# Kernel optimization log

Hardware: AMD Instinct MI355X
Metric: run time of the kernel (lower is better)

## Reference

```python
import jax, jax.numpy as jnp
import numpy as np

B, S, D, H, HG, W, DFF = 2, 4096, 1024, 16, 2, 128, 4096
NEG = -1e30  # stands in for -inf in the original masking (exp underflows to exactly 0)


def _chunk(x, w):
    # overlapping chunks of size 2w with hop w (tf.signal.frame equivalent)
    b, s, d = x.shape
    blocks = x.reshape(b, s // w, w, d)
    return jnp.concatenate([blocks[:, :-1], blocks[:, 1:]], axis=2)  # [b, s//w-1, 2w, d]


def _sliding_scores(q, k, w):
    # q,k: [BH, S, dh] (q pre-scaled). Returns banded scores [BH, S, 2w+1].
    bh, s, d = q.shape
    c = s // w - 1
    attn = jnp.einsum('bcxd,bcyd->bcxy', _chunk(q, w), _chunk(k, w))  # [bh,c,2w,2w]
    # pad one row then reshape: the skew trick from the source (_pad_and_transpose_last_two_dims)
    dca = jnp.pad(attn, ((0, 0), (0, 0), (0, 1), (0, 0))).reshape(bh, c, 2 * w, 2 * w + 1)
    up = jnp.concatenate([dca[:, :, :w, :w + 1], dca[:, -1:, w:, :w + 1]], axis=1)          # [bh,c+1,w,w+1]
    first = jnp.roll(dca, shift=(1, w), axis=(2, 3))[:, :1, :w, :w]                          # first-chunk lower triangle
    low = jnp.concatenate([first, dca[:, :, -(w + 1):-1, w + 1:]], axis=1)                   # [bh,c+1,w,w]
    return jnp.concatenate([low, up], axis=-1).reshape(bh, s, 2 * w + 1)


def _invalid_mask(s, w):
    # _mask_invalid_locations: mask band positions that fall outside [0, S)
    m = jnp.tril(jnp.ones((w, w + 1), jnp.float32))[::-1]
    m = jnp.pad(m, ((0, s - w), (0, w)))
    return (m + m[::-1, ::-1]) > 0  # [s, 2w+1]


def _sliding_value(p, v, w):
    # p: [BH, S, 2w+1] band probs, v: [BH, S, dh] -> [BH, S, dh]
    bh, s, kk = p.shape
    d = v.shape[-1]
    c = s // w
    cp = jnp.pad(p.reshape(bh, c, w, kk), ((0, 0), (0, 0), (0, 0), (0, w + 1)))
    # pad-and-diagonalize skew: row r shifted right by r -> aligns band with 3w value window
    cp = cp.reshape(bh, c, w * (3 * w + 2))[:, :, :-w].reshape(bh, c, w, 3 * w + 1)[:, :, :, :-1]
    pv = jnp.pad(v, ((0, 0), (w, w), (0, 0))).reshape(bh, c + 2, w, d)
    cv = jnp.concatenate([pv[:, :-2], pv[:, 1:-1], pv[:, 2:]], axis=2)  # [bh,c,3w,d]
    return jnp.einsum('bcwk,bckd->bcwd', cp, cv).reshape(bh, s, d)


def _layernorm(x, g, b):
    mu = jnp.mean(x, -1, keepdims=True)
    var = jnp.mean(jnp.square(x - mu), -1, keepdims=True)
    return (x - mu) * jax.lax.rsqrt(var + 1e-6) * g + b


def setup_inputs() -> dict:
    key = jax.random.key(0)
    ks = jax.random.split(key, 8)
    dense = lambda k, i, o: 0.02 * jax.random.normal(k, (i, o), jnp.float32)
    return {
        'x': jax.random.normal(ks[0], (B, S, D), jnp.float32),
        'mask': jnp.zeros((B, 1, 1, S), jnp.float32),
        'wq_k': dense(ks[1], D, D), 'wq_b': jnp.zeros((D,), jnp.float32),
        'wk_k': dense(ks[2], D, D), 'wk_b': jnp.zeros((D,), jnp.float32),
        'wv_k': dense(ks[3], D, D), 'wv_b': jnp.zeros((D,), jnp.float32),
        'wo_k': dense(ks[4], D, D), 'wo_b': jnp.zeros((D,), jnp.float32),
        'ffn_w1': dense(ks[5], D, DFF), 'ffn_b1': jnp.zeros((DFF,), jnp.float32),
        'ffn_w2': dense(ks[6], DFF, D), 'ffn_b2': jnp.zeros((D,), jnp.float32),
        'ln1_g': jnp.ones((D,), jnp.float32), 'ln1_b': jnp.zeros((D,), jnp.float32),
        'ln2_g': jnp.ones((D,), jnp.float32), 'ln2_b': jnp.zeros((D,), jnp.float32),
    }


def reference(x, mask, wq_k, wq_b, wk_k, wk_b, wv_k, wv_b, wo_k, wo_b,
              ffn_w1, ffn_b1, ffn_w2, ffn_b2, ln1_g, ln1_b, ln2_g, ln2_b):
    dh = D // H
    hl = H - HG
    split = lambda t: t.reshape(B, S, H, dh).transpose(0, 2, 1, 3)  # [B,H,S,dh]
    q, k, v = split(x @ wq_k + wq_b), split(x @ wk_k + wk_b), split(x @ wv_k + wv_b)
    scale = 1.0 / jnp.sqrt(jnp.float32(dh))
    # ---- local (sliding-window) heads ----
    ql = (q[:, :hl] * scale).reshape(B * hl, S, dh)
    kl = k[:, :hl].reshape(B * hl, S, dh)
    vl = v[:, :hl].reshape(B * hl, S, dh)
    scores = _sliding_scores(ql, kl, W)
    scores = jnp.where(_invalid_mask(S, W)[None], NEG, scores)
    out_l = _sliding_value(jax.nn.softmax(scores, axis=-1), vl, W).reshape(B, hl, S, dh)
    # ---- global heads (full attention, graph_mask=None branch) ----
    logits = jnp.einsum('bhqd,bhkd->bhqk', q[:, hl:], k[:, hl:]) * scale + mask * (-1000.0)
    out_g = jnp.einsum('bhqk,bhkd->bhqd', jax.nn.softmax(logits, axis=-1), v[:, hl:])
    # ---- merge heads, output proj, residual + LN, FFN (leaky_relu alpha=0.2 = tf default) ----
    attn = jnp.concatenate([out_l, out_g], axis=1).transpose(0, 2, 1, 3).reshape(B, S, D)
    out1 = _layernorm(x + attn @ wo_k + wo_b, ln1_g, ln1_b)
    h = jax.nn.leaky_relu(out1 @ ffn_w1 + ffn_b1, negative_slope=0.2)
    return _layernorm(out1 + h @ ffn_w2 + ffn_b2, ln2_g, ln2_b)
```

## Files before the change

### kernel.cpp

```cpp
#include <hip/hip_runtime.h>
#include <hip/hip_bf16.h>

typedef unsigned short u16;
typedef unsigned int u32;
typedef __attribute__((ext_vector_type(8))) short short8;
typedef __attribute__((ext_vector_type(8))) unsigned short ushort8v;
typedef __attribute__((ext_vector_type(4))) unsigned short ushort4v;
typedef __attribute__((ext_vector_type(4))) float f32x4;

static constexpr int B_ = 2, S_ = 4096, D_ = 1024, H_ = 16, HG_ = 2, W_ = 128, DFF_ = 4096;
static constexpr int HL_ = H_ - HG_;
static constexpr int M_ = B_ * S_;
static constexpr int NCH_ = 4;

static __device__ __forceinline__ u16 f2b(float f) {
    u32 u = __builtin_bit_cast(u32, f);
    u32 r = (u + 0x7fffu + ((u >> 16) & 1u)) >> 16;
    return (u16)r;
}
static __device__ __forceinline__ float b2f(u16 b) {
    return __builtin_bit_cast(float, (u32)b << 16);
}

__global__ __launch_bounds__(256) void k_f32_to_bf16(const float* __restrict__ src,
                                                     u16* __restrict__ dst, int n4) {
    int i = blockIdx.x * 256 + threadIdx.x;
    if (i >= n4) return;
    float4 v = reinterpret_cast<const float4*>(src)[i];
    ushort4v o; o[0] = f2b(v.x); o[1] = f2b(v.y); o[2] = f2b(v.z); o[3] = f2b(v.w);
    reinterpret_cast<ushort4v*>(dst)[i] = o;
}

__global__ __launch_bounds__(256) void k_transpose_bf16(const float* __restrict__ src,
                                                        u16* __restrict__ dst,
                                                        int K, int N, int ro) {
    __shared__ float tile[32][33];
    const int tx = threadIdx.x & 31, ty = threadIdx.x >> 5;
    const int bx = blockIdx.x, by = blockIdx.y;
#pragma unroll
    for (int jj = 0; jj < 4; ++jj) {
        int kk = by * 32 + ty + jj * 8;
        int nn = bx * 32 + tx;
        tile[ty + jj * 8][tx] = src[(size_t)kk * N + nn];
    }
    __syncthreads();
#pragma unroll
    for (int jj = 0; jj < 4; ++jj) {
        int nn = bx * 32 + ty + jj * 8;
        int kk = by * 32 + tx;
        dst[(size_t)(ro + nn) * K + kk] = f2b(tile[tx][ty + jj * 8]);
    }
}

__global__ __launch_bounds__(256) void k_transpose_v(const u16* __restrict__ qkv,
                                                     u16* __restrict__ vT) {
    __shared__ u16 tile[32][33];
    const int tx = threadIdx.x & 31, ty = threadIdx.x >> 5;
    const int s0 = blockIdx.x * 32;
    const int d0 = blockIdx.y * 32;
    const int bh = blockIdx.z;
    const int b = bh >> 4, h = bh & 15;
#pragma unroll
    for (int jj = 0; jj < 4; ++jj) {
        int srow = s0 + ty + jj * 8;
        tile[ty + jj * 8][tx] = qkv[(size_t)(b * S_ + srow) * 3072 + 2048 + h * 64 + d0 + tx];
    }
    __syncthreads();
#pragma unroll
    for (int jj = 0; jj < 4; ++jj) {
        int d = d0 + ty + jj * 8;
        vT[(size_t)((b * H_ + h) * 64 + d) * S_ + s0 + tx] = tile[tx][ty + jj * 8];
    }
}

__global__ void k_pack_bias3(const float* __restrict__ a, const float* __restrict__ b,
                             const float* __restrict__ c, float* __restrict__ dst) {
    int i = blockIdx.x * 256 + threadIdx.x;
    if (i >= 3072) return;
    dst[i] = i < 1024 ? a[i] : (i < 2048 ? b[i - 1024] : c[i - 2048]);
}

#define GLDS16(gp, lp) __builtin_amdgcn_global_load_lds( \
    (const __attribute__((address_space(1))) void*)(gp),  \
    (__attribute__((address_space(3))) void*)(lp), 16, 0, 0)

template <bool LEAKY, bool OUTF, bool OUTB>
__global__ __launch_bounds__(256) void k_gemm(const u16* __restrict__ A, const u16* __restrict__ Bt,
                                              const float* __restrict__ bias,
                                              float* __restrict__ Cf, u16* __restrict__ Cb,
                                              int M, int N, int K) {
    __shared__ __align__(16) u16 lA[128 * 32];
    __shared__ __align__(16) u16 lB[128 * 32];
    const int tid = threadIdx.x;
    const int lane = tid & 63, wave = tid >> 6;
    const int wr = wave >> 1, wc = wave & 1;
    const int m0 = blockIdx.x * 128, n0 = blockIdx.y * 128;

    f32x4 acc[4][4];
#pragma unroll
    for (int i = 0; i < 4; ++i)
#pragma unroll
        for (int j = 0; j < 4; ++j)
#pragma unroll
            for (int e = 0; e < 4; ++e) acc[i][j][e] = 0.f;

    const int arow = tid >> 2;
    const int acol = (tid & 3) * 8;
    const int koff = (lane >> 4) * 8;
    const int rbase = wr * 64 + (lane & 15);
    const int cbase = wc * 64 + (lane & 15);

    for (int k0 = 0; k0 < K; k0 += 32) {
        __syncthreads();
        {
            const u16* ga0 = A + (size_t)(m0 + arow) * K + k0 + acol;
            const u16* ga1 = A + (size_t)(m0 + 64 + arow) * K + k0 + acol;
            GLDS16(ga0, lA + wave * 512);
            GLDS16(ga1, lA + 2048 + wave * 512);
            const u16* gb0 = Bt + (size_t)(n0 + arow) * K + k0 + acol;
            const u16* gb1 = Bt + (size_t)(n0 + 64 + arow) * K + k0 + acol;
            GLDS16(gb0, lB + wave * 512);
            GLDS16(gb1, lB + 2048 + wave * 512);
        }
        __syncthreads();

        short8 af[4], bfr[4];
#pragma unroll
        for (int mi = 0; mi < 4; ++mi)
            af[mi] = *reinterpret_cast<const short8*>(&lA[(rbase + mi * 16) * 32 + koff]);
#pragma unroll
        for (int ni = 0; ni < 4; ++ni)
            bfr[ni] = *reinterpret_cast<const short8*>(&lB[(cbase + ni * 16) * 32 + koff]);
        __builtin_amdgcn_s_setprio(1);
#pragma unroll
        for (int mi = 0; mi < 4; ++mi)
#pragma unroll
            for (int ni = 0; ni < 4; ++ni)
                acc[mi][ni] = __builtin_amdgcn_mfma_f32_16x16x32_bf16(af[mi], bfr[ni], acc[mi][ni], 0, 0, 0);
        __builtin_amdgcn_s_setprio(0);
    }

#pragma unroll
    for (int mi = 0; mi < 4; ++mi) {
        const int rowb = m0 + wr * 64 + mi * 16 + (lane >> 4) * 4;
#pragma unroll
        for (int ni = 0; ni < 4; ++ni) {
            const int col = n0 + wc * 64 + ni * 16 + (lane & 15);
            const float bs = bias[col];
#pragma unroll
            for (int j = 0; j < 4; ++j) {
                float v = acc[mi][ni][j] + bs;
                if (LEAKY) v = v > 0.f ? v : 0.2f * v;
                const size_t idx = (size_t)(rowb + j) * N + col;
                if (OUTF) Cf[idx] = v;
                if (OUTB) Cb[idx] = f2b(v);
            }
        }
    }
}

__global__ __launch_bounds__(256) void k_attn_local(const u16* __restrict__ qkv,
                                                    const u16* __restrict__ vT,
                                                    u16* __restrict__ out) {
    __shared__ __align__(16) u16 Kl[64][72];
    __shared__ __align__(16) u16 Vl[64][72];
    __shared__ __align__(16) u16 Pl[4][1024];
    const int tid = threadIdx.x, lane = tid & 63, wave = tid >> 6;
    const int c = lane & 15, g = lane >> 4;
    const int b = blockIdx.z, h = blockIdx.y;
    const int q0 = blockIdx.x * 64;
    const int qrow = q0 + wave * 16 + c;

    short8 qf[2];
    {
        const u16* qp = qkv + (size_t)(b * S_ + qrow) * 3072 + h * 64 + g * 8;
        qf[0] = *reinterpret_cast<const short8*>(qp);
        qf[1] = *reinterpret_cast<const short8*>(qp + 32);
    }

    f32x4 acc[4];
#pragma unroll
    for (int dt = 0; dt < 4; ++dt)
#pragma unroll
        for (int j = 0; j < 4; ++j) acc[dt][j] = 0.f;
    float mrow = -1e30f, lrow = 0.f;

    const int t_lo = max(0, q0 - W_) >> 6;
    const int t_hi = min(S_ - 1, q0 + 63 + W_) >> 6;
    u16* pw = Pl[wave];

    for (int t = t_lo; t <= t_hi; ++t) {
        __syncthreads();
#pragma unroll
        for (int it = 0; it < 2; ++it) {
            int L = it * 256 + tid;
            int r = L >> 3, cb = (L & 7) * 8;
            *reinterpret_cast<ushort8v*>(&Kl[r][cb]) =
                *reinterpret_cast<const ushort8v*>(&qkv[(size_t)(b * S_ + t * 64 + r) * 3072 + 1024 + h * 64 + cb]);
            *reinterpret_cast<ushort8v*>(&Vl[r][cb]) =
                *reinterpret_cast<const ushort8v*>(&vT[(size_t)((b * H_ + h) * 64 + r) * S_ + t * 64 + cb]);
        }
        __syncthreads();

        f32x4 s[4];
#pragma unroll
        for (int nt = 0; nt < 4; ++nt)
#pragma unroll
            for (int j = 0; j < 4; ++j) s[nt][j] = 0.f;
        __builtin_amdgcn_s_setprio(1);
#pragma unroll
        for (int kc = 0; kc < 2; ++kc) {
#pragma unroll
            for (int nt = 0; nt < 4; ++nt) {
                short8 kf = *reinterpret_cast<const short8*>(&Kl[nt * 16 + c][kc * 32 + g * 8]);
                s[nt] = __builtin_amdgcn_mfma_f32_16x16x32_bf16(kf, qf[kc], s[nt], 0, 0, 0);
            }
        }
        __builtin_amdgcn_s_setprio(0);

        float p[4][4];
        float tmax = -1e30f;
#pragma unroll
        for (int nt = 0; nt < 4; ++nt)
#pragma unroll
            for (int j = 0; j < 4; ++j) {
                float sv = s[nt][j] * 0.125f;
                int key = t * 64 + nt * 16 + 4 * g + j;
                bool val = (key >= qrow - W_) && (key <= qrow + W_);
                sv = val ? sv : -1e30f;
                p[nt][j] = sv;
                tmax = fmaxf(tmax, sv);
            }
        tmax = fmaxf(tmax, __shfl_xor(tmax, 16));
        tmax = fmaxf(tmax, __shfl_xor(tmax, 32));
        float mnew = fmaxf(mrow, tmax);
        float fac = __expf(mrow - mnew);
        mrow = mnew;
        float psum = 0.f;
#pragma unroll
        for (int nt = 0; nt < 4; ++nt)
#pragma unroll
            for (int j = 0; j < 4; ++j) {
                p[nt][j] = __expf(p[nt][j] - mnew);
                psum += p[nt][j];
            }
        lrow = lrow * fac + psum;
#pragma unroll
        for (int dt = 0; dt < 4; ++dt)
#pragma unroll
            for (int j = 0; j < 4; ++j) acc[dt][j] *= fac;

#pragma unroll
        for (int nt = 0; nt < 4; ++nt)
#pragma unroll
            for (int jp = 0; jp < 2; ++jp) {
                u32 pk = (u32)f2b(p[nt][2 * jp]) | ((u32)f2b(p[nt][2 * jp + 1]) << 16);
                int byteoff = (c << 7) + ((nt * 32 + 8 * g + 4 * jp) ^ ((c & 7) << 4));
                *reinterpret_cast<u32*>(reinterpret_cast<char*>(pw) + byteoff) = pk;
            }
        asm volatile("s_waitcnt lgkmcnt(0)" ::: "memory");

        __builtin_amdgcn_s_setprio(1);
#pragma unroll
        for (int h2 = 0; h2 < 2; ++h2) {
            int rb = (c << 7) + ((h2 * 64 + g * 16) ^ ((c & 7) << 4));
            short8 pa = *reinterpret_cast<const short8*>(reinterpret_cast<char*>(pw) + rb);
#pragma unroll
            for (int dt = 0; dt < 4; ++dt) {
                short8 vf = *reinterpret_cast<const short8*>(&Vl[dt * 16 + c][h2 * 32 + g * 8]);
                acc[dt] = __builtin_amdgcn_mfma_f32_16x16x32_bf16(vf, pa, acc[dt], 0, 0, 0);
            }
        }
        __builtin_amdgcn_s_setprio(0);
    }

    float lfull = lrow + __shfl_xor(lrow, 16);
    lfull += __shfl_xor(lfull, 32);
    const float rinv = 1.0f / lfull;

#pragma unroll
    for (int dt = 0; dt < 4; ++dt) {
        u32 w0 = (u32)f2b(acc[dt][0] * rinv) | ((u32)f2b(acc[dt][1] * rinv) << 16);
        u32 w1 = (u32)f2b(acc[dt][2] * rinv) | ((u32)f2b(acc[dt][3] * rinv) << 16);
        uint2 wv; wv.x = w0; wv.y = w1;
        *reinterpret_cast<uint2*>(out + (size_t)(b * S_ + qrow) * 1024 + h * 64 + dt * 16 + 4 * g) = wv;
    }
}

__global__ __launch_bounds__(256) void k_attn_global_part(const u16* __restrict__ qkv,
                                                          const u16* __restrict__ vT,
                                                          const float* __restrict__ mask,
                                                          float* __restrict__ po,
                                                          float* __restrict__ ml) {
    __shared__ __align__(16) u16 Kl[64][72];
    __shared__ __align__(16) u16 Vl[64][72];
    __shared__ __align__(16) u16 Pl[4][1024];
    __shared__ float maskl[64];
    const int tid = threadIdx.x, lane = tid & 63, wave = tid >> 6;
    const int c = lane & 15, g = lane >> 4;
    const int b = blockIdx.z;
    const int hh = blockIdx.y >> 2, ch = blockIdx.y & 3;
    const int h = HL_ + hh;
    const int q0 = blockIdx.x * 64;
    const int qrow = q0 + wave * 16 + c;

    short8 qf[2];
    {
        const u16* qp = qkv + (size_t)(b * S_ + qrow) * 3072 + h * 64 + g * 8;
        qf[0] = *reinterpret_cast<const short8*>(qp);
        qf[1] = *reinterpret_cast<const short8*>(qp + 32);
    }

    f32x4 acc[4];
#pragma unroll
    for (int dt = 0; dt < 4; ++dt)
#pragma unroll
        for (int j = 0; j < 4; ++j) acc[dt][j] = 0.f;
    float mrow = -1e30f, lrow = 0.f;
    u16* pw = Pl[wave];

    const int t_lo = ch * (S_ / 64 / NCH_), t_hi = t_lo + (S_ / 64 / NCH_) - 1;
    for (int t = t_lo; t <= t_hi; ++t) {
        __syncthreads();
#pragma unroll
        for (int it = 0; it < 2; ++it) {
            int L = it * 256 + tid;
            int r = L >> 3, cb = (L & 7) * 8;
            *reinterpret_cast<ushort8v*>(&Kl[r][cb]) =
                *reinterpret_cast<const ushort8v*>(&qkv[(size_t)(b * S_ + t * 64 + r) * 3072 + 1024 + h * 64 + cb]);
            *reinterpret_cast<ushort8v*>(&Vl[r][cb]) =
                *reinterpret_cast<const ushort8v*>(&vT[(size_t)((b * H_ + h) * 64 + r) * S_ + t * 64 + cb]);
        }
        if (tid < 64) maskl[tid] = mask[b * S_ + t * 64 + tid] * (-1000.0f);
        __syncthreads();

        f32x4 s[4];
#pragma unroll
        for (int nt = 0; nt < 4; ++nt)
#pragma unroll
            for (int j = 0; j < 4; ++j) s[nt][j] = 0.f;
        __builtin_amdgcn_s_setprio(1);
#pragma unroll
        for (int kc = 0; kc < 2; ++kc) {
#pragma unroll
            for (int nt = 0; nt < 4; ++nt) {
                short8 kf = *reinterpret_cast<const short8*>(&Kl[nt * 16 + c][kc * 32 + g * 8]);
                s[nt] = __builtin_amdgcn_mfma_f32_16x16x32_bf16(kf, qf[kc], s[nt], 0, 0, 0);
            }
        }
        __builtin_amdgcn_s_setprio(0);

        float p[4][4];
        float tmax = -1e30f;
#pragma unroll
        for (int nt = 0; nt < 4; ++nt)
#pragma unroll
            for (int j = 0; j < 4; ++j) {
                float sv = s[nt][j] * 0.125f + maskl[nt * 16 + 4 * g + j];
                p[nt][j] = sv;
                tmax = fmaxf(tmax, sv);
            }
        tmax = fmaxf(tmax, __shfl_xor(tmax, 16));
        tmax = fmaxf(tmax, __shfl_xor(tmax, 32));
        float mnew = fmaxf(mrow, tmax);
        float fac = __expf(mrow - mnew);
        mrow = mnew;
        float psum = 0.f;
#pragma unroll
        for (int nt = 0; nt < 4; ++nt)
#pragma unroll
            for (int j = 0; j < 4; ++j) {
                p[nt][j] = __expf(p[nt][j] - mnew);
                psum += p[nt][j];
            }
        lrow = lrow * fac + psum;
#pragma unroll
        for (int dt = 0; dt < 4; ++dt)
#pragma unroll
            for (int j = 0; j < 4; ++j) acc[dt][j] *= fac;

#pragma unroll
        for (int nt = 0; nt < 4; ++nt)
#pragma unroll
            for (int jp = 0; jp < 2; ++jp) {
                u32 pk = (u32)f2b(p[nt][2 * jp]) | ((u32)f2b(p[nt][2 * jp + 1]) << 16);
                int byteoff = (c << 7) + ((nt * 32 + 8 * g + 4 * jp) ^ ((c & 7) << 4));
                *reinterpret_cast<u32*>(reinterpret_cast<char*>(pw) + byteoff) = pk;
            }
        asm volatile("s_waitcnt lgkmcnt(0)" ::: "memory");

        __builtin_amdgcn_s_setprio(1);
#pragma unroll
        for (int h2 = 0; h2 < 2; ++h2) {
            int rb = (c << 7) + ((h2 * 64 + g * 16) ^ ((c & 7) << 4));
            short8 pa = *reinterpret_cast<const short8*>(reinterpret_cast<char*>(pw) + rb);
#pragma unroll
            for (int dt = 0; dt < 4; ++dt) {
                short8 vf = *reinterpret_cast<const short8*>(&Vl[dt * 16 + c][h2 * 32 + g * 8]);
                acc[dt] = __builtin_amdgcn_mfma_f32_16x16x32_bf16(vf, pa, acc[dt], 0, 0, 0);
            }
        }
        __builtin_amdgcn_s_setprio(0);
    }

    float lfull = lrow + __shfl_xor(lrow, 16);
    lfull += __shfl_xor(lfull, 32);

    float* po_blk = po + ((((size_t)(b * HG_ + hh) * NCH_ + ch) * (S_ / 64) + blockIdx.x) * 4096);
    const int ql = wave * 16 + c;
#pragma unroll
    for (int dt = 0; dt < 4; ++dt)
        *reinterpret_cast<f32x4*>(po_blk + ql * 64 + dt * 16 + 4 * g) = acc[dt];
    if (g == 0) {
        size_t mb = (((size_t)(b * HG_ + hh) * NCH_ + ch) * S_ + q0 + ql) * 2;
        ml[mb] = mrow;
        ml[mb + 1] = lfull;
    }
}

__global__ __launch_bounds__(256) void k_attn_merge(const float* __restrict__ po,
                                                    const float* __restrict__ ml,
                                                    u16* __restrict__ out) {
    const int qb = blockIdx.x, hh = blockIdx.y, b = blockIdx.z;
    const int t = threadIdx.x;
    const int ql = t >> 2, d0 = (t & 3) * 16;
    const int q = qb * 64 + ql;

    float mv[NCH_], lv[NCH_];
    float M = -1e30f;
#pragma unroll
    for (int ch = 0; ch < NCH_; ++ch) {
        size_t mb = (((size_t)(b * HG_ + hh) * NCH_ + ch) * S_ + q) * 2;
        mv[ch] = ml[mb];
        lv[ch] = ml[mb + 1];
        M = fmaxf(M, mv[ch]);
    }
    float wch[NCH_], L = 0.f;
#pragma unroll
    for (int ch = 0; ch < NCH_; ++ch) {
        wch[ch] = __expf(mv[ch] - M);
        L += wch[ch] * lv[ch];
    }
    const float rL = 1.0f / L;

    float o[16];
#pragma unroll
    for (int i = 0; i < 16; ++i) o[i] = 0.f;
#pragma unroll
    for (int ch = 0; ch < NCH_; ++ch) {
        const float* pb = po + ((((size_t)(b * HG_ + hh) * NCH_ + ch) * (S_ / 64) + qb) * 4096) + ql * 64 + d0;
        const float w = wch[ch];
#pragma unroll
        for (int i = 0; i < 4; ++i) {
            float4 v = reinterpret_cast<const float4*>(pb)[i];
            o[4 * i + 0] += w * v.x; o[4 * i + 1] += w * v.y;
            o[4 * i + 2] += w * v.z; o[4 * i + 3] += w * v.w;
        }
    }
    ushort8v r0, r1;
#pragma unroll
    for (int i = 0; i < 8; ++i) { r0[i] = f2b(o[i] * rL); r1[i] = f2b(o[8 + i] * rL); }
    u16* op = out + (size_t)(b * S_ + q) * 1024 + (HL_ + hh) * 64 + d0;
    *reinterpret_cast<ushort8v*>(op) = r0;
    *reinterpret_cast<ushort8v*>(op + 8) = r1;
}

__global__ __launch_bounds__(256) void k_ln(const float* __restrict__ base, const float* __restrict__ delta,
                                            const float* __restrict__ g, const float* __restrict__ bt,
                                            float* __restrict__ outf, u16* __restrict__ outb) {
    __shared__ float red[8];
    const int row = blockIdx.x, tid = threadIdx.x;
    const int lane = tid & 63, wave = tid >> 6;
    float4 xb = reinterpret_cast<const float4*>(base + (size_t)row * 1024)[tid];
    float4 xd = reinterpret_cast<const float4*>(delta + (size_t)row * 1024)[tid];
    float x0 = xb.x + xd.x, x1 = xb.y + xd.y, x2 = xb.z + xd.z, x3 = xb.w + xd.w;
    float s = x0 + x1 + x2 + x3;
#pragma unroll
    for (int off = 32; off >= 1; off >>= 1) s += __shfl_xor(s, off);
    if (lane == 0) red[wave] = s;
    __syncthreads();
    float mu = (red[0] + red[1] + red[2] + red[3]) * (1.f / 1024.f);
    float d0 = x0 - mu, d1 = x1 - mu, d2 = x2 - mu, d3 = x3 - mu;
    float s2 = d0 * d0 + d1 * d1 + d2 * d2 + d3 * d3;
#pragma unroll
    for (int off = 32; off >= 1; off >>= 1) s2 += __shfl_xor(s2, off);
    if (lane == 0) red[4 + wave] = s2;
    __syncthreads();
    float var = (red[4] + red[5] + red[6] + red[7]) * (1.f / 1024.f);
    float rs = rsqrtf(var + 1e-6f);
    float4 gv = reinterpret_cast<const float4*>(g)[tid];
    float4 bv = reinterpret_cast<const float4*>(bt)[tid];
    float o0 = d0 * rs * gv.x + bv.x;
    float o1 = d1 * rs * gv.y + bv.y;
    float o2 = d2 * rs * gv.z + bv.z;
    float o3 = d3 * rs * gv.w + bv.w;
    if (outf) {
        float4 ov; ov.x = o0; ov.y = o1; ov.z = o2; ov.w = o3;
        reinterpret_cast<float4*>(outf + (size_t)row * 1024)[tid] = ov;
    }
    if (outb) {
        ushort4v ob; ob[0] = f2b(o0); ob[1] = f2b(o1); ob[2] = f2b(o2); ob[3] = f2b(o3);
        reinterpret_cast<ushort4v*>(outb + (size_t)row * 1024)[tid] = ob;
    }
}

extern "C" void kernel_launch(void* const* d_in, const int* in_sizes, int n_in,
                              void* d_out, int out_size, void* d_ws, size_t ws_size,
                              hipStream_t stream) {
    const float* x    = (const float*)d_in[0];
    const float* mask = (const float*)d_in[1];
    const float* wq   = (const float*)d_in[2];
    const float* wq_b = (const float*)d_in[3];
    const float* wk   = (const float*)d_in[4];
    const float* wk_b = (const float*)d_in[5];
    const float* wv   = (const float*)d_in[6];
    const float* wv_b = (const float*)d_in[7];
    const float* wo   = (const float*)d_in[8];
    const float* wo_b = (const float*)d_in[9];
    const float* w1   = (const float*)d_in[10];
    const float* b1   = (const float*)d_in[11];
    const float* w2   = (const float*)d_in[12];
    const float* b2   = (const float*)d_in[13];
    const float* ln1g = (const float*)d_in[14];
    const float* ln1b = (const float*)d_in[15];
    const float* ln2g = (const float*)d_in[16];
    const float* ln2b = (const float*)d_in[17];
    float* out = (float*)d_out;

    char* ws = (char*)d_ws;
    const size_t MB = 1024ull * 1024ull;
    u16*   qkv_b  = (u16*)(ws + 0);
    u16*   h_b    = (u16*)(ws + 0);
    u16*   vTb    = (u16*)(ws + 64 * MB);
    float* ybuf   = (float*)(ws + 64 * MB);
    float* po     = (float*)(ws + 96 * MB);
    float* ml     = (float*)(ws + 113 * MB);
    float* out1   = (float*)(ws + 96 * MB);
    u16*   xb     = (u16*)(ws + 128 * MB);
    u16*   attn_b = (u16*)(ws + 128 * MB);
    u16*   out1_b = (u16*)(ws + 128 * MB);
    u16*   wT     = (u16*)(ws + 144 * MB);
    float* bias3  = (float*)(ws + 152 * MB);

    const dim3 tb(256);

    k_f32_to_bf16<<<(M_ * D_ / 4 + 255) / 256, tb, 0, stream>>>(x, xb, M_ * D_ / 4);
    k_transpose_bf16<<<dim3(32, 32), tb, 0, stream>>>(wq, wT, 1024, 1024, 0);
    k_transpose_bf16<<<dim3(32, 32), tb, 0, stream>>>(wk, wT, 1024, 1024, 1024);
    k_transpose_bf16<<<dim3(32, 32), tb, 0, stream>>>(wv, wT, 1024, 1024, 2048);
    k_pack_bias3<<<12, tb, 0, stream>>>(wq_b, wk_b, wv_b, bias3);
    k_gemm<false, false, true><<<dim3(M_ / 128, 3072 / 128), tb, 0, stream>>>(
        xb, wT, bias3, nullptr, qkv_b, M_, 3072, 1024);
    k_transpose_v<<<dim3(S_ / 32, 2, B_ * H_), tb, 0, stream>>>(qkv_b, vTb);
    k_attn_local<<<dim3(S_ / 64, HL_, B_), tb, 0, stream>>>(qkv_b, vTb, attn_b);
    k_attn_global_part<<<dim3(S_ / 64, HG_ * NCH_, B_), tb, 0, stream>>>(qkv_b, vTb, mask, po, ml);
    k_attn_merge<<<dim3(S_ / 64, HG_, B_), tb, 0, stream>>>(po, ml, attn_b);
    k_transpose_bf16<<<dim3(32, 32), tb, 0, stream>>>(wo, wT, 1024, 1024, 0);
    k_gemm<false, true, false><<<dim3(M_ / 128, 1024 / 128), tb, 0, stream>>>(
        attn_b, wT, wo_b, ybuf, nullptr, M_, 1024, 1024);
    k_ln<<<M_, tb, 0, stream>>>(x, ybuf, ln1g, ln1b, out1, out1_b);
    k_transpose_bf16<<<dim3(128, 32), tb, 0, stream>>>(w1, wT, 1024, 4096, 0);
    k_gemm<true, false, true><<<dim3(M_ / 128, 4096 / 128), tb, 0, stream>>>(
        out1_b, wT, b1, nullptr, h_b, M_, 4096, 1024);
    k_transpose_bf16<<<dim3(32, 128), tb, 0, stream>>>(w2, wT, 4096, 1024, 0);
    k_gemm<false, true, false><<<dim3(M_ / 128, 1024 / 128), tb, 0, stream>>>(
        h_b, wT, b2, ybuf, nullptr, M_, 1024, 4096);
    k_ln<<<M_, tb, 0, stream>>>(out1, ybuf, ln2g, ln2b, out, nullptr);
}
```

Measured before the change: 433.6 us.

## Double GEMM K-tile to 64 and XOR-swizzle LDS layout

The GEMM kernel now stages 64-wide K slices of A and B into LDS per iteration instead of 32. That halves the number of barrier pairs per K loop and runs two MFMA sub-steps per staged tile. The LDS layout uses an XOR swizzle of 16-byte column groups by row, so fragment reads avoid bank conflicts. LDS usage doubles to 32 KB per block, which may reduce occupancy.

```diff
diff --git a/kernel.cpp b/kernel.cpp
--- a/kernel.cpp
+++ b/kernel.cpp
@@ -89,8 +89,8 @@
                                               const float* __restrict__ bias,
                                               float* __restrict__ Cf, u16* __restrict__ Cb,
                                               int M, int N, int K) {
-    __shared__ __align__(16) u16 lA[128 * 32];
-    __shared__ __align__(16) u16 lB[128 * 32];
+    __shared__ __align__(16) u16 lA[128 * 64];
+    __shared__ __align__(16) u16 lB[128 * 64];
     const int tid = threadIdx.x;
     const int lane = tid & 63, wave = tid >> 6;
     const int wr = wave >> 1, wc = wave & 1;
@@ -104,40 +104,48 @@
 #pragma unroll
             for (int e = 0; e < 4; ++e) acc[i][j][e] = 0.f;
 
-    const int arow = tid >> 2;
-    const int acol = (tid & 3) * 8;
-    const int koff = (lane >> 4) * 8;
-    const int rbase = wr * 64 + (lane & 15);
-    const int cbase = wc * 64 + (lane & 15);
-
-    for (int k0 = 0; k0 < K; k0 += 32) {
+    const int srow = tid >> 3;
+    const int sgc = (tid & 7) ^ (srow & 7);
+    const int c = lane & 15, g4 = lane >> 4;
+
+    const u16* gA = A + (size_t)(m0 + srow) * K + sgc * 8;
+    const u16* gB = Bt + (size_t)(n0 + srow) * K + sgc * 8;
+
+    const char* lAc = reinterpret_cast<const char*>(lA);
+    const char* lBc = reinterpret_cast<const char*>(lB);
+
+    for (int k0 = 0; k0 < K; k0 += 64) {
         __syncthreads();
-        {
-            const u16* ga0 = A + (size_t)(m0 + arow) * K + k0 + acol;
-            const u16* ga1 = A + (size_t)(m0 + 64 + arow) * K + k0 + acol;
-            GLDS16(ga0, lA + wave * 512);
-            GLDS16(ga1, lA + 2048 + wave * 512);
-            const u16* gb0 = Bt + (size_t)(n0 + arow) * K + k0 + acol;
-            const u16* gb1 = Bt + (size_t)(n0 + 64 + arow) * K + k0 + acol;
-            GLDS16(gb0, lB + wave * 512);
-            GLDS16(gb1, lB + 2048 + wave * 512);
+#pragma unroll
+        for (int j = 0; j < 4; ++j) {
+            GLDS16(gA + k0 + (size_t)j * 32 * K, lA + j * 2048 + wave * 512);
+            GLDS16(gB + k0 + (size_t)j * 32 * K, lB + j * 2048 + wave * 512);
         }
         __syncthreads();
 
-        short8 af[4], bfr[4];
-#pragma unroll
-        for (int mi = 0; mi < 4; ++mi)
-            af[mi] = *reinterpret_cast<const short8*>(&lA[(rbase + mi * 16) * 32 + koff]);
-#pragma unroll
-        for (int ni = 0; ni < 4; ++ni)
-            bfr[ni] = *reinterpret_cast<const short8*>(&lB[(cbase + ni * 16) * 32 + koff]);
-        __builtin_amdgcn_s_setprio(1);
-#pragma unroll
-        for (int mi = 0; mi < 4; ++mi)
-#pragma unroll
-            for (int ni = 0; ni < 4; ++ni)
-                acc[mi][ni] = __builtin_amdgcn_mfma_f32_16x16x32_bf16(af[mi], bfr[ni], acc[mi][ni], 0, 0, 0);
-        __builtin_amdgcn_s_setprio(0);
+#pragma unroll
+        for (int ks = 0; ks < 2; ++ks) {
+            short8 af[4], bfr[4];
+#pragma unroll
+            for (int mi = 0; mi < 4; ++mi) {
+                const int r = wr * 64 + mi * 16 + c;
+                const int gl = (ks * 4 + g4) ^ (c & 7);
+                af[mi] = *reinterpret_cast<const short8*>(lAc + r * 128 + gl * 16);
+            }
+#pragma unroll
+            for (int ni = 0; ni < 4; ++ni) {
+                const int r = wc * 64 + ni * 16 + c;
+                const int gl = (ks * 4 + g4) ^ (c & 7);
+                bfr[ni] = *reinterpret_cast<const short8*>(lBc + r * 128 + gl * 16);
+            }
+            __builtin_amdgcn_s_setprio(1);
+#pragma unroll
+            for (int mi = 0; mi < 4; ++mi)
+#pragma unroll
+                for (int ni = 0; ni < 4; ++ni)
+                    acc[mi][ni] = __builtin_amdgcn_mfma_f32_16x16x32_bf16(af[mi], bfr[ni], acc[mi][ni], 0, 0, 0);
+            __builtin_amdgcn_s_setprio(0);
+        }
     }
 
 #pragma unroll
```

New measurement: 402.4 us. 7.2% less time.
